# Optimization experiments

Hardware: AMD Instinct MI355X
Metric: run time of the kernel (lower is better)

The kernel has to match this reference:

```python
import jax, jax.numpy as jnp
import numpy as np

ITER_STEPS = 2
NODE_DIM = 512

def _rmv(t, m, value):
    # allennlp.replace_masked_values: keep t where mask nonzero, else value
    return jnp.where(m != 0, t, value)

def setup_inputs() -> dict:
    key = jax.random.key(0)
    ks = jax.random.split(key, 24)
    B, R, C, D, d = 16, 64, 64, 2048, NODE_DIM
    inp = {
        "question_node": jax.random.normal(ks[0], (B, d), jnp.float32),
        "table_row_header_nodes": jax.random.normal(ks[1], (B, R, d), jnp.float32),
        "table_col_header_nodes": jax.random.normal(ks[2], (B, C, d), jnp.float32),
        "table_data_cell_nodes": jax.random.normal(ks[3], (B, D, d), jnp.float32),
        "table_row_header_index_mask": jax.random.randint(ks[4], (B, R), 0, 2, jnp.int32),
        "table_col_header_index_mask": jax.random.randint(ks[5], (B, C), 0, 2, jnp.int32),
        "table_data_cell_index_mask": jax.random.randint(ks[6], (B, D), 0, 2, jnp.int32),
        "same_row_data_cell_relation": jax.random.randint(ks[7], (B, D, D), 0, 2, jnp.int32),
        "same_col_data_cell_relation": jax.random.randint(ks[8], (B, D, D), 0, 2, jnp.int32),
        "data_cell_row_rel": jax.random.randint(ks[9], (B, R, D), 0, 2, jnp.int32),
        "data_cell_col_rel": jax.random.randint(ks[10], (B, C, D), 0, 2, jnp.int32),
        # parameters (Linear(in,out) stores weight [out,in]; y = x @ W.T)
        "w_node": jax.random.normal(ks[11], (1, d), jnp.float32) / np.sqrt(d),
        "w_row_data_cell": jax.random.normal(ks[12], (d, d), jnp.float32) / np.sqrt(d),
        "w_col_data_cell": jax.random.normal(ks[13], (d, d), jnp.float32) / np.sqrt(d),
        "w_data_cell_row": jax.random.normal(ks[14], (d, d), jnp.float32) / np.sqrt(d),
        "w_data_cell_col": jax.random.normal(ks[15], (d, d), jnp.float32) / np.sqrt(d),
        "w_same_row": jax.random.normal(ks[16], (d, d), jnp.float32) / np.sqrt(d),
        "w_same_col": jax.random.normal(ks[17], (d, d), jnp.float32) / np.sqrt(d),
        "w_row_question": jax.random.normal(ks[18], (d, d), jnp.float32) / np.sqrt(d),
        "w_col_question": jax.random.normal(ks[19], (d, d), jnp.float32) / np.sqrt(d),
    }
    return inp


def reference(question_node, table_row_header_nodes, table_col_header_nodes,
              table_data_cell_nodes, table_row_header_index_mask,
              table_col_header_index_mask, table_data_cell_index_mask,
              same_row_data_cell_relation, same_col_data_cell_relation,
              data_cell_row_rel, data_cell_col_rel,
              w_node, w_row_data_cell, w_col_data_cell, w_data_cell_row,
              w_data_cell_col, w_same_row, w_same_col, w_row_question,
              w_col_question):
    rm = table_row_header_index_mask.astype(jnp.float32)   # [B,R]
    cm = table_col_header_index_mask.astype(jnp.float32)   # [B,C]
    dm = table_data_cell_index_mask.astype(jnp.float32)    # [B,D]

    # masked relation graphs (0/1 float)
    rh_dc_graph = data_cell_row_rel.astype(jnp.float32) * (rm[:, :, None] * dm[:, None, :])   # [B,R,D]
    ch_dc_graph = data_cell_col_rel.astype(jnp.float32) * (cm[:, :, None] * dm[:, None, :])   # [B,C,D]
    dc_dc_mask = dm[:, :, None] * dm[:, None, :]
    same_row_graph = same_row_data_cell_relation.astype(jnp.float32) * dc_dc_mask             # [B,D,D]
    same_col_graph = same_col_data_cell_relation.astype(jnp.float32) * dc_dc_mask             # [B,D,D]

    rh_num = rh_dc_graph.sum(-1)                                  # [B,R]
    rh_num = _rmv(rh_num + 1.0, (rh_num >= 1), 1.0)
    ch_num = ch_dc_graph.sum(-1)                                  # [B,C]
    ch_num = _rmv(ch_num + 1.0, (ch_num >= 1), 1.0)
    dc_num = (same_row_graph.sum(-1) + same_col_graph.sum(-1)
              + rh_dc_graph.sum(1) + ch_dc_graph.sum(1))          # [B,D]
    dc_num = _rmv(dc_num, (dc_num >= 1), 1.0)

    rh = table_row_header_nodes
    ch = table_col_header_nodes
    dc = table_data_cell_nodes
    q = question_node

    for _ in range(ITER_STEPS):
        rh_w = jax.nn.sigmoid(rh @ w_node.T)[..., 0]   # [B,R]
        ch_w = jax.nn.sigmoid(ch @ w_node.T)[..., 0]   # [B,C]
        dc_w = jax.nn.sigmoid(dc @ w_node.T)[..., 0]   # [B,D]

        rh_dc_info = dc @ w_row_data_cell.T            # [B,D,d]
        ch_dc_info = dc @ w_col_data_cell.T            # [B,D,d]
        rh_q_info = (q @ w_row_question.T)[:, None, :] * rm[:, :, None]  # [B,R,d]
        ch_q_info = (q @ w_col_question.T)[:, None, :] * cm[:, :, None]  # [B,C,d]
        same_row_info = dc @ w_same_row.T              # [B,D,d]
        same_col_info = dc @ w_same_col.T              # [B,D,d]
        dc_rh_info = rh @ w_data_cell_row.T            # [B,R,d]
        dc_ch_info = ch @ w_data_cell_col.T            # [B,C,d]

        # gated adjacency weights: source-node sigmoid gate masked by graph
        rh_dc_weight = jnp.where(rh_dc_graph != 0, dc_w[:, None, :], 0.0)         # [B,R,D]
        ch_dc_weight = jnp.where(ch_dc_graph != 0, dc_w[:, None, :], 0.0)         # [B,C,D]
        same_row_weight = jnp.where(same_row_graph != 0, dc_w[:, None, :], 0.0)   # [B,D,D]
        same_col_weight = jnp.where(same_col_graph != 0, dc_w[:, None, :], 0.0)   # [B,D,D]
        dc_rh_weight = jnp.where(jnp.swapaxes(rh_dc_graph, 1, 2) != 0, rh_w[:, None, :], 0.0)  # [B,D,R]
        dc_ch_weight = jnp.where(jnp.swapaxes(ch_dc_graph, 1, 2) != 0, ch_w[:, None, :], 0.0)  # [B,D,C]

        rh_dc_agg = jnp.matmul(rh_dc_weight, rh_dc_info)        # [B,R,d]
        ch_dc_agg = jnp.matmul(ch_dc_weight, ch_dc_info)        # [B,C,d]
        same_row_agg = jnp.matmul(same_row_weight, same_row_info)  # [B,D,d]
        same_col_agg = jnp.matmul(same_col_weight, same_col_info)  # [B,D,d]
        dc_rh_agg = jnp.matmul(dc_rh_weight, dc_rh_info)        # [B,D,d]
        dc_ch_agg = jnp.matmul(dc_ch_weight, dc_ch_info)        # [B,D,d]

        agg_rh = (rh_dc_agg + rh_q_info) / rh_num[:, :, None]
        agg_ch = (ch_dc_agg + ch_q_info) / ch_num[:, :, None]
        # NOTE: faithful to source bug: dc_ch_agg appears twice, same_col_agg unused
        agg_dc = (same_row_agg + dc_ch_agg + dc_rh_agg + dc_ch_agg) / dc_num[:, :, None]

        rh = jax.nn.relu(agg_rh)
        ch = jax.nn.relu(agg_ch)
        dc = jax.nn.relu(agg_dc)

    return (rh, ch, dc)
```

## Files before the change

kernel.cpp:

```cpp
#include <hip/hip_runtime.h>
#include <math.h>

#define NB 16
#define NR 64
#define NCOL 64
#define ND 2048
#define DIM 512

typedef __attribute__((ext_vector_type(4))) float f32x4;
typedef __attribute__((ext_vector_type(8))) short bf16x8;
typedef __attribute__((ext_vector_type(8))) unsigned short us8;

#define OFF_RHNUM  0L
#define OFF_CHNUM  1024L
#define OFF_DCNUM  2048L
#define OFF_RHW    34816L
#define OFF_CHW    35840L
#define OFF_QROW   36864L
#define OFF_QCOL   45056L
#define OFF_PRER   53248L
#define OFF_PREC   577536L
#define OFF_INFORC 1101824L
#define OFF_BITS   2150400L
#define OFF_DCS    4247552L
#define OFF_PROJ   21024768L
#define WS_FLOATS  37801984L

__device__ inline void bsplit(float v, unsigned short& h, unsigned short& l) {
    unsigned uv = __float_as_uint(v);
    unsigned hb = (uv + 0x7FFFu + ((uv >> 16) & 1u)) >> 16;
    h = (unsigned short)hb;
    float lo = v - __uint_as_float(hb << 16);
    unsigned lv = __float_as_uint(lo);
    l = (unsigned short)((lv + 0x7FFFu + ((lv >> 16) & 1u)) >> 16);
}

__device__ inline unsigned spread4(unsigned x) {
    x = (x | (x << 12)) & 0x000F000Fu;
    x = (x | (x << 6))  & 0x03030303u;
    x = (x | (x << 3))  & 0x11111111u;
    return x;
}

__device__ inline void mfma_phase2(const unsigned short* Aexp, const unsigned short* Bhi,
                                   const unsigned short* Blo, int wm, int wn, int lane,
                                   f32x4 acc[4][4])
{
    #pragma unroll
    for (int ks = 0; ks < 2; ks++) {
        bf16x8 af[4], bh[4], bl[4];
        #pragma unroll
        for (int i = 0; i < 4; i++) {
            int rr = wm * 64 + i * 16 + (lane & 15);
            int cc = (ks * 4 + (lane >> 4)) ^ (rr & 7);
            af[i] = *(const bf16x8*)((const char*)Aexp + rr * 128 + cc * 16);
            int nn = wn * 64 + i * 16 + (lane & 15);
            int c2 = (ks * 4 + (lane >> 4)) ^ (nn & 7);
            bh[i] = *(const bf16x8*)((const char*)Bhi + nn * 128 + c2 * 16);
            bl[i] = *(const bf16x8*)((const char*)Blo + nn * 128 + c2 * 16);
        }
        #pragma unroll
        for (int mi = 0; mi < 4; mi++)
            #pragma unroll
            for (int ni = 0; ni < 4; ni++) {
                acc[mi][ni] = __builtin_amdgcn_mfma_f32_16x16x32_bf16(af[mi], bh[ni], acc[mi][ni], 0, 0, 0);
                acc[mi][ni] = __builtin_amdgcn_mfma_f32_16x16x32_bf16(af[mi], bl[ni], acc[mi][ni], 0, 0, 0);
            }
    }
}

__global__ __launch_bounds__(256) void k_gate_rc(
    const float* __restrict__ rh, const float* __restrict__ ch,
    const int* __restrict__ rm, const int* __restrict__ cm,
    const float* __restrict__ wnode,
    float* __restrict__ rh_w, float* __restrict__ ch_w)
{
    int wave = threadIdx.x >> 6, lane = threadIdx.x & 63;
    int idx = blockIdx.x * 4 + wave;
    const float* xrow; float* outw; int mval;
    if (idx < NB * NR) {
        int b = idx >> 6, r = idx & 63;
        xrow = rh + ((long)b * NR + r) * DIM; mval = rm[b * NR + r]; outw = rh_w + b * NR + r;
    } else {
        int tt = idx - NB * NR; int b = tt >> 6, c = tt & 63;
        xrow = ch + ((long)b * NCOL + c) * DIM; mval = cm[b * NCOL + c]; outw = ch_w + b * NCOL + c;
    }
    const float4* px = (const float4*)xrow;
    const float4* pw = (const float4*)wnode;
    float4 xa = px[lane * 2], xb = px[lane * 2 + 1];
    float4 wa = pw[lane * 2], wb = pw[lane * 2 + 1];
    float s = xa.x * wa.x + xa.y * wa.y + xa.z * wa.z + xa.w * wa.w
            + xb.x * wb.x + xb.y * wb.y + xb.z * wb.z + xb.w * wb.w;
    #pragma unroll
    for (int o = 32; o > 0; o >>= 1) s += __shfl_xor(s, o, 64);
    if (lane == 0) {
        float g = 1.f / (1.f + expf(-s));
        *outw = mval ? g : 0.f;
    }
}

__global__ __launch_bounds__(256) void k_split(
    const float* __restrict__ src, const float* __restrict__ wnode, const int* __restrict__ dmask,
    unsigned short* __restrict__ dhi, unsigned short* __restrict__ dlo,
    unsigned short* __restrict__ thi, unsigned short* __restrict__ tlo)
{
    int b = blockIdx.y, j0 = blockIdx.x * 16;
    __shared__ float X[16 * 512];
    __shared__ float scs[16];
    int t = threadIdx.x;
    int r = t >> 4, u = t & 15;
    const float* row = src + ((long)b * ND + j0 + r) * DIM;
    float part = 0.f;
    #pragma unroll
    for (int i = 0; i < 8; i++) {
        int col = i * 64 + u * 4;
        float4 v = *(const float4*)(row + col);
        float4 w = *(const float4*)(wnode + col);
        part += v.x * w.x + v.y * w.y + v.z * w.z + v.w * w.w;
        *(float4*)&X[r * 512 + (col ^ ((r & 7) * 4))] = v;
    }
    part += __shfl_xor(part, 1, 64);
    part += __shfl_xor(part, 2, 64);
    part += __shfl_xor(part, 4, 64);
    part += __shfl_xor(part, 8, 64);
    if (u == 0) {
        float g = 1.f / (1.f + expf(-part));
        scs[r] = (dmask[(long)b * ND + j0 + r] != 0) ? g : 0.f;
    }
    __syncthreads();
    {
        float s = scs[r];
        long ob = ((long)b * ND + j0 + r) * DIM + u * 32;
        #pragma unroll
        for (int g = 0; g < 4; g++) {
            us8 ph, pl;
            #pragma unroll
            for (int e = 0; e < 8; e++) {
                int cc = u * 32 + g * 8 + e;
                float v = X[r * 512 + (cc ^ ((r & 7) * 4))] * s;
                unsigned short hh, ll; bsplit(v, hh, ll);
                ph[e] = hh; pl[e] = ll;
            }
            *(us8*)(dhi + ob + g * 8) = ph;
            *(us8*)(dlo + ob + g * 8) = pl;
        }
    }
    #pragma unroll
    for (int h = 0; h < 2; h++) {
        int n = t + h * 256;
        us8 ph0, ph1, pl0, pl1;
        #pragma unroll
        for (int rr = 0; rr < 16; rr++) {
            float v = X[rr * 512 + (n ^ ((rr & 7) * 4))] * scs[rr];
            unsigned short hh, ll; bsplit(v, hh, ll);
            if (rr < 8) { ph0[rr] = hh; pl0[rr] = ll; }
            else        { ph1[rr - 8] = hh; pl1[rr - 8] = ll; }
        }
        long ob = ((long)b * DIM + n) * ND + j0;
        *(us8*)(thi + ob) = ph0; *(us8*)(thi + ob + 8) = ph1;
        *(us8*)(tlo + ob) = pl0; *(us8*)(tlo + ob + 8) = pl1;
    }
}

__global__ __launch_bounds__(256) void k_wsplit(
    const float* __restrict__ w, unsigned short* __restrict__ whi, unsigned short* __restrict__ wlo)
{
    long i = ((long)blockIdx.x * 256 + threadIdx.x) * 8;
    float4 a = *(const float4*)(w + i), b4 = *(const float4*)(w + i + 4);
    float v[8] = {a.x, a.y, a.z, a.w, b4.x, b4.y, b4.z, b4.w};
    us8 ph, pl;
    #pragma unroll
    for (int t = 0; t < 8; t++) {
        unsigned short hh, ll; bsplit(v[t], hh, ll);
        ph[t] = hh; pl[t] = ll;
    }
    *(us8*)(whi + i) = ph;
    *(us8*)(wlo + i) = pl;
}

__global__ __launch_bounds__(256) void k_q(
    const float* __restrict__ q, const float* __restrict__ wrq, const float* __restrict__ wcq,
    float* __restrict__ qrow, float* __restrict__ qcol)
{
    int b = blockIdx.z;
    const float* W = blockIdx.y ? wcq : wrq;
    float* out = blockIdx.y ? qcol : qrow;
    int wave = threadIdx.x >> 6, lane = threadIdx.x & 63;
    int n = blockIdx.x * 4 + wave;
    const float4* qp = (const float4*)(q + (long)b * DIM);
    const float4* wp = (const float4*)(W + (long)n * DIM);
    float4 a0 = qp[lane * 2], a1 = qp[lane * 2 + 1];
    float4 w0 = wp[lane * 2], w1 = wp[lane * 2 + 1];
    float s = a0.x * w0.x + a0.y * w0.y + a0.z * w0.z + a0.w * w0.w
            + a1.x * w1.x + a1.y * w1.y + a1.z * w1.z + a1.w * w1.w;
    #pragma unroll
    for (int o = 32; o > 0; o >>= 1) s += __shfl_xor(s, o, 64);
    if (lane == 0) out[(long)b * DIM + n] = s;
}

__global__ __launch_bounds__(256) void k_bits(
    const int* __restrict__ sr, const int* __restrict__ sc, const int* __restrict__ dmask,
    unsigned* __restrict__ bits, float* __restrict__ dcnum)
{
    long bi0 = (long)blockIdx.x * 2;
    int b = (int)(bi0 >> 11);
    int wave = threadIdx.x >> 6, lane = threadIdx.x & 63;
    const int4* dm4 = (const int4*)(dmask + (long)b * ND);
    int4 vs[2][2], vc[2][2], vd[2];
    #pragma unroll
    for (int h = 0; h < 2; h++) {
        int vidx = wave * 128 + h * 64 + lane;
        vd[h] = dm4[vidx];
        #pragma unroll
        for (int r = 0; r < 2; r++) {
            vs[r][h] = ((const int4*)(sr + (bi0 + r) * ND))[vidx];
            vc[r][h] = ((const int4*)(sc + (bi0 + r) * ND))[vidx];
        }
    }
    int dmi0 = dmask[bi0], dmi1 = dmask[bi0 + 1];
    __shared__ int red[2][4];
    #pragma unroll
    for (int r = 0; r < 2; r++) {
        int dmi = r ? dmi1 : dmi0;
        unsigned* brow = bits + (bi0 + r) * 64;
        int cnt = 0;
        #pragma unroll
        for (int h = 0; h < 2; h++) {
            int4 s4 = vs[r][h], c4 = vc[r][h], d4 = vd[h];
            bool d0 = dmi && d4.x, d1 = dmi && d4.y, d2 = dmi && d4.z, d3 = dmi && d4.w;
            unsigned long long m0 = __ballot(d0 && s4.x);
            unsigned long long m1 = __ballot(d1 && s4.y);
            unsigned long long m2 = __ballot(d2 && s4.z);
            unsigned long long m3 = __ballot(d3 && s4.w);
            unsigned long long n0 = __ballot(d0 && c4.x);
            unsigned long long n1 = __ballot(d1 && c4.y);
            unsigned long long n2 = __ballot(d2 && c4.z);
            unsigned long long n3 = __ballot(d3 && c4.w);
            cnt += __popcll(m0) + __popcll(m1) + __popcll(m2) + __popcll(m3)
                 + __popcll(n0) + __popcll(n1) + __popcll(n2) + __popcll(n3);
            if (lane < 8) {
                unsigned w = spread4((unsigned)(m0 >> (8 * lane)) & 0xFFu)
                           | (spread4((unsigned)(m1 >> (8 * lane)) & 0xFFu) << 1)
                           | (spread4((unsigned)(m2 >> (8 * lane)) & 0xFFu) << 2)
                           | (spread4((unsigned)(m3 >> (8 * lane)) & 0xFFu) << 3);
                brow[wave * 16 + h * 8 + lane] = w;
            }
        }
        if (lane == 0) red[r][wave] = cnt;
    }
    __syncthreads();
    if (threadIdx.x < 2) {
        int s = red[threadIdx.x][0] + red[threadIdx.x][1] + red[threadIdx.x][2] + red[threadIdx.x][3];
        dcnum[bi0 + threadIdx.x] = (float)s;
    }
}

__global__ __launch_bounds__(256) void k_rcnum(
    const int* __restrict__ rel_rd, const int* __restrict__ rel_cd,
    const int* __restrict__ rm, const int* __restrict__ cm, const int* __restrict__ dmask,
    float* __restrict__ rh_num, float* __restrict__ ch_num)
{
    int wave = threadIdx.x >> 6, lane = threadIdx.x & 63;
    long idx = (long)blockIdx.x * 4 + wave;
    const int* row; int mval; float* out; const int* dmb;
    if (idx < NB * NR) {
        int b = (int)(idx >> 6), r = (int)(idx & 63);
        row = rel_rd + ((long)b * NR + r) * ND; mval = rm[b * NR + r];
        out = rh_num + b * NR + r; dmb = dmask + (long)b * ND;
    } else {
        long tt = idx - NB * NR; int b = (int)(tt >> 6), c = (int)(tt & 63);
        row = rel_cd + ((long)b * NCOL + c) * ND; mval = cm[b * NCOL + c];
        out = ch_num + b * NCOL + c; dmb = dmask + (long)b * ND;
    }
    int cnt = 0;
    for (int rr = 0; rr < 32; rr++) {
        int j = rr * 64 + lane;
        cnt += (row[j] != 0 && dmb[j] != 0) ? 1 : 0;
    }
    #pragma unroll
    for (int o = 32; o > 0; o >>= 1) cnt += __shfl_xor(cnt, o, 64);
    if (lane == 0) {
        float s = mval ? (float)cnt : 0.f;
        *out = (s >= 1.f) ? (s + 1.f) : 1.f;
    }
}

__global__ __launch_bounds__(256) void k_dcnum_final(
    const int* __restrict__ rel_rd, const int* __restrict__ rel_cd,
    const int* __restrict__ rm, const int* __restrict__ cm, const int* __restrict__ dmask,
    float* __restrict__ dcnum)
{
    int b = blockIdx.y;
    int j = blockIdx.x * 256 + threadIdx.x;
    const int* rd = rel_rd + (long)b * NR * ND;
    const int* cd = rel_cd + (long)b * NCOL * ND;
    const int* rmb = rm + b * NR;
    const int* cmb = cm + b * NCOL;
    int cnt = 0;
    for (int r = 0; r < NR; r++)  cnt += (rd[(long)r * ND + j] != 0 && rmb[r] != 0) ? 1 : 0;
    for (int c = 0; c < NCOL; c++) cnt += (cd[(long)c * ND + j] != 0 && cmb[c] != 0) ? 1 : 0;
    float add = (dmask[(long)b * ND + j] != 0) ? (float)cnt : 0.f;
    float tv = dcnum[(long)b * ND + j] + add;
    dcnum[(long)b * ND + j] = (tv >= 1.f) ? tv : 1.f;
}

__global__ __launch_bounds__(256) void gemm_info(
    const float* __restrict__ A, long sA,
    const float* __restrict__ W,
    unsigned short* __restrict__ ihiT, unsigned short* __restrict__ iloT, int hoff,
    const float* __restrict__ rowscale, float alpha)
{
    int b = blockIdx.z;
    int n0 = blockIdx.x * 64;
    __shared__ float As[32][68], Ws[32][68];
    float acc[4][4] = {};
    int tx = threadIdx.x & 15, ty = threadIdx.x >> 4;
    int lm = threadIdx.x >> 2, lk = (threadIdx.x & 3) * 8;
    const float* Ab = A + (long)b * sA;
    for (int k0 = 0; k0 < DIM; k0 += 32) {
        const float4* pa = (const float4*)(Ab + (long)lm * DIM + k0 + lk);
        float4 va0 = pa[0], va1 = pa[1];
        const float4* pw = (const float4*)(W + (long)(n0 + lm) * DIM + k0 + lk);
        float4 vw0 = pw[0], vw1 = pw[1];
        As[lk + 0][lm] = va0.x; As[lk + 1][lm] = va0.y; As[lk + 2][lm] = va0.z; As[lk + 3][lm] = va0.w;
        As[lk + 4][lm] = va1.x; As[lk + 5][lm] = va1.y; As[lk + 6][lm] = va1.z; As[lk + 7][lm] = va1.w;
        Ws[lk + 0][lm] = vw0.x; Ws[lk + 1][lm] = vw0.y; Ws[lk + 2][lm] = vw0.z; Ws[lk + 3][lm] = vw0.w;
        Ws[lk + 4][lm] = vw1.x; Ws[lk + 5][lm] = vw1.y; Ws[lk + 6][lm] = vw1.z; Ws[lk + 7][lm] = vw1.w;
        __syncthreads();
        #pragma unroll
        for (int kk = 0; kk < 32; kk++) {
            float4 av = *(const float4*)&As[kk][ty * 4];
            float4 wv = *(const float4*)&Ws[kk][tx * 4];
            float a[4] = {av.x, av.y, av.z, av.w};
            float w[4] = {wv.x, wv.y, wv.z, wv.w};
            #pragma unroll
            for (int mi = 0; mi < 4; mi++)
                #pragma unroll
                for (int ni = 0; ni < 4; ni++)
                    acc[mi][ni] += a[mi] * w[ni];
        }
        __syncthreads();
    }
    #pragma unroll
    for (int mi = 0; mi < 4; mi++) {
        int gm = ty * 4 + mi;
        float scv = alpha * rowscale[(long)b * 64 + gm];
        #pragma unroll
        for (int ni = 0; ni < 4; ni++) {
            float v = scv * acc[mi][ni];
            unsigned short hh, ll; bsplit(v, hh, ll);
            long off = ((long)b * DIM + n0 + tx * 4 + ni) * 128 + hoff + gm;
            ihiT[off] = hh; iloT[off] = ll;
        }
    }
}

__global__ __launch_bounds__(256) void gemm_head(
    const float* __restrict__ A, long sA,
    const float* __restrict__ W,
    float* __restrict__ C, long sC,
    const int* __restrict__ mrow, const float* __restrict__ addvec,
    const float* __restrict__ rownum)
{
    int b = blockIdx.z;
    int n0 = blockIdx.x * 64;
    __shared__ float As[32][68], Ws[32][68];
    float acc[4][4] = {};
    int tx = threadIdx.x & 15, ty = threadIdx.x >> 4;
    int lm = threadIdx.x >> 2, lk = (threadIdx.x & 3) * 8;
    const float* Ab = A + (long)b * sA;
    for (int k0 = 0; k0 < DIM; k0 += 32) {
        const float4* pa = (const float4*)(Ab + (long)lm * DIM + k0 + lk);
        float4 va0 = pa[0], va1 = pa[1];
        const float4* pw = (const float4*)(W + (long)(n0 + lm) * DIM + k0 + lk);
        float4 vw0 = pw[0], vw1 = pw[1];
        As[lk + 0][lm] = va0.x; As[lk + 1][lm] = va0.y; As[lk + 2][lm] = va0.z; As[lk + 3][lm] = va0.w;
        As[lk + 4][lm] = va1.x; As[lk + 5][lm] = va1.y; As[lk + 6][lm] = va1.z; As[lk + 7][lm] = va1.w;
        Ws[lk + 0][lm] = vw0.x; Ws[lk + 1][lm] = vw0.y; Ws[lk + 2][lm] = vw0.z; Ws[lk + 3][lm] = vw0.w;
        Ws[lk + 4][lm] = vw1.x; Ws[lk + 5][lm] = vw1.y; Ws[lk + 6][lm] = vw1.z; Ws[lk + 7][lm] = vw1.w;
        __syncthreads();
        #pragma unroll
        for (int kk = 0; kk < 32; kk++) {
            float4 av = *(const float4*)&As[kk][ty * 4];
            float4 wv = *(const float4*)&Ws[kk][tx * 4];
            float a[4] = {av.x, av.y, av.z, av.w};
            float w[4] = {wv.x, wv.y, wv.z, wv.w};
            #pragma unroll
            for (int mi = 0; mi < 4; mi++)
                #pragma unroll
                for (int ni = 0; ni < 4; ni++)
                    acc[mi][ni] += a[mi] * w[ni];
        }
        __syncthreads();
    }
    #pragma unroll
    for (int mi = 0; mi < 4; mi++) {
        int gm = ty * 4 + mi;
        float mq = (mrow[(long)b * 64 + gm] != 0) ? 1.f : 0.f;
        float inv = 1.f / rownum[(long)b * 64 + gm];
        float4 o;
        float* vo = (float*)&o;
        #pragma unroll
        for (int ni = 0; ni < 4; ni++) {
            float tv = (acc[mi][ni] + mq * addvec[(long)b * DIM + n0 + tx * 4 + ni]) * inv;
            vo[ni] = fmaxf(tv, 0.f);
        }
        *(float4*)(C + (long)b * sC + (long)gm * DIM + n0 + tx * 4) = o;
    }
}

__global__ __launch_bounds__(256) void k_pre_rc_mfma(
    const int* __restrict__ rel_rd, const int* __restrict__ rel_cd,
    const unsigned short* __restrict__ thi, const unsigned short* __restrict__ tlo,
    const int* __restrict__ rm, const int* __restrict__ cm,
    float* __restrict__ pre_r, float* __restrict__ pre_c)
{
    int b = blockIdx.y, n0 = blockIdx.x * 64;
    __shared__ unsigned short Aexp[128 * 64];
    __shared__ unsigned short Bhi[64 * 64], Blo[64 * 64];
    int tid = threadIdx.x, lane = tid & 63, wid = tid >> 6;
    int wm = wid >> 1, wn = wid & 1;
    int arow = tid >> 1, aseg = tid & 1;
    const int* relrow = (arow < 64)
        ? rel_rd + ((long)b * 64 + arow) * ND
        : rel_cd + ((long)b * 64 + arow - 64) * ND;
    int bn = tid >> 2, bq = tid & 3;
    const unsigned short* bsrc_h = thi + ((long)b * DIM + n0 + bn) * ND;
    const unsigned short* bsrc_l = tlo + ((long)b * DIM + n0 + bn) * ND;

    f32x4 acc[4][2];
    #pragma unroll
    for (int i = 0; i < 4; i++)
        #pragma unroll
        for (int j = 0; j < 2; j++)
            acc[i][j] = (f32x4){0.f, 0.f, 0.f, 0.f};

    for (int k0 = 0; k0 < ND; k0 += 64) {
        {
            const int4* pa = (const int4*)(relrow + k0 + aseg * 32);
            #pragma unroll
            for (int p = 0; p < 4; p++) {
                int4 v0 = pa[2 * p], v1 = pa[2 * p + 1];
                uint4 qv;
                qv.x = (v0.x ? 0x3F80u : 0u) | (v0.y ? 0x3F800000u : 0u);
                qv.y = (v0.z ? 0x3F80u : 0u) | (v0.w ? 0x3F800000u : 0u);
                qv.z = (v1.x ? 0x3F80u : 0u) | (v1.y ? 0x3F800000u : 0u);
                qv.w = (v1.z ? 0x3F80u : 0u) | (v1.w ? 0x3F800000u : 0u);
                int c = (aseg * 4 + p) ^ (arow & 7);
                *(uint4*)((char*)Aexp + arow * 128 + c * 16) = qv;
            }
        }
        {
            const uint4* ph = (const uint4*)(bsrc_h + k0 + bq * 16);
            const uint4* pl = (const uint4*)(bsrc_l + k0 + bq * 16);
            #pragma unroll
            for (int s = 0; s < 2; s++) {
                int c = (bq * 2 + s) ^ (bn & 7);
                *(uint4*)((char*)Bhi + bn * 128 + c * 16) = ph[s];
                *(uint4*)((char*)Blo + bn * 128 + c * 16) = pl[s];
            }
        }
        __syncthreads();
        #pragma unroll
        for (int ks = 0; ks < 2; ks++) {
            bf16x8 af[4], bh[2], bl[2];
            #pragma unroll
            for (int i = 0; i < 4; i++) {
                int rr = wm * 64 + i * 16 + (lane & 15);
                int cc = (ks * 4 + (lane >> 4)) ^ (rr & 7);
                af[i] = *(bf16x8*)((char*)Aexp + rr * 128 + cc * 16);
            }
            #pragma unroll
            for (int i = 0; i < 2; i++) {
                int nn = wn * 32 + i * 16 + (lane & 15);
                int c2 = (ks * 4 + (lane >> 4)) ^ (nn & 7);
                bh[i] = *(bf16x8*)((char*)Bhi + nn * 128 + c2 * 16);
                bl[i] = *(bf16x8*)((char*)Blo + nn * 128 + c2 * 16);
            }
            #pragma unroll
            for (int mi = 0; mi < 4; mi++)
                #pragma unroll
                for (int ni = 0; ni < 2; ni++) {
                    acc[mi][ni] = __builtin_amdgcn_mfma_f32_16x16x32_bf16(af[mi], bh[ni], acc[mi][ni], 0, 0, 0);
                    acc[mi][ni] = __builtin_amdgcn_mfma_f32_16x16x32_bf16(af[mi], bl[ni], acc[mi][ni], 0, 0, 0);
                }
        }
        __syncthreads();
    }
    const int* msk = wm ? cm : rm;
    float* outp = wm ? pre_c : pre_r;
    #pragma unroll
    for (int mi = 0; mi < 4; mi++) {
        int grow = mi * 16 + (lane >> 4) * 4;
        #pragma unroll
        for (int ni = 0; ni < 2; ni++) {
            int gcol = n0 + wn * 32 + ni * 16 + (lane & 15);
            #pragma unroll
            for (int r = 0; r < 4; r++) {
                int rrow = grow + r;
                float scv = (msk[b * 64 + rrow] != 0) ? 1.f : 0.f;
                outp[((long)b * 64 + rrow) * DIM + gcol] = scv * acc[mi][ni][r];
            }
        }
    }
}

__global__ __launch_bounds__(256) void k_proj_mfma(
    const unsigned short* __restrict__ whi, const unsigned short* __restrict__ wlo,
    const unsigned short* __restrict__ dhi, const unsigned short* __restrict__ dlo,
    unsigned short* __restrict__ phi, unsigned short* __restrict__ plo)
{
    int flat = blockIdx.x;
    int tile = (flat & 7) * 128 + (flat >> 3);
    int b = tile >> 6;
    int rem = tile & 63;
    int m0 = (rem >> 4) * 128;
    int n0 = (rem & 15) * 128;

    __shared__ unsigned short SM[4 * 128 * 64];
    unsigned short* Ahi = SM;
    unsigned short* Alo = SM + 128 * 64;
    unsigned short* Bhi = SM + 2 * 128 * 64;
    unsigned short* Blo = SM + 3 * 128 * 64;

    int tid = threadIdx.x;
    int lane = tid & 63, wid = tid >> 6;
    int wm = wid >> 1, wn = wid & 1;
    int srow = tid >> 1, sseg = tid & 1;

    f32x4 acc[4][4];
    #pragma unroll
    for (int i = 0; i < 4; i++)
        #pragma unroll
        for (int j = 0; j < 4; j++)
            acc[i][j] = (f32x4){0.f, 0.f, 0.f, 0.f};

    for (int k0 = 0; k0 < DIM; k0 += 64) {
        {
            const uint4* ph = (const uint4*)(whi + (long)(m0 + srow) * DIM + k0 + sseg * 32);
            const uint4* pl = (const uint4*)(wlo + (long)(m0 + srow) * DIM + k0 + sseg * 32);
            #pragma unroll
            for (int s = 0; s < 4; s++) {
                int c = (sseg * 4 + s) ^ (srow & 7);
                *(uint4*)((char*)Ahi + srow * 128 + c * 16) = ph[s];
                *(uint4*)((char*)Alo + srow * 128 + c * 16) = pl[s];
            }
        }
        {
            const uint4* ph = (const uint4*)(dhi + ((long)b * ND + n0 + srow) * DIM + k0 + sseg * 32);
            const uint4* pl = (const uint4*)(dlo + ((long)b * ND + n0 + srow) * DIM + k0 + sseg * 32);
            #pragma unroll
            for (int s = 0; s < 4; s++) {
                int c = (sseg * 4 + s) ^ (srow & 7);
                *(uint4*)((char*)Bhi + srow * 128 + c * 16) = ph[s];
                *(uint4*)((char*)Blo + srow * 128 + c * 16) = pl[s];
            }
        }
        __syncthreads();
        #pragma unroll
        for (int ks = 0; ks < 2; ks++) {
            bf16x8 ah[4], al[4], bh[4], bl[4];
            #pragma unroll
            for (int i = 0; i < 4; i++) {
                int rr = wm * 64 + i * 16 + (lane & 15);
                int cc = (ks * 4 + (lane >> 4)) ^ (rr & 7);
                ah[i] = *(bf16x8*)((char*)Ahi + rr * 128 + cc * 16);
                al[i] = *(bf16x8*)((char*)Alo + rr * 128 + cc * 16);
                int nn = wn * 64 + i * 16 + (lane & 15);
                int c2 = (ks * 4 + (lane >> 4)) ^ (nn & 7);
                bh[i] = *(bf16x8*)((char*)Bhi + nn * 128 + c2 * 16);
                bl[i] = *(bf16x8*)((char*)Blo + nn * 128 + c2 * 16);
            }
            #pragma unroll
            for (int mi = 0; mi < 4; mi++)
                #pragma unroll
                for (int ni = 0; ni < 4; ni++) {
                    acc[mi][ni] = __builtin_amdgcn_mfma_f32_16x16x32_bf16(ah[mi], bh[ni], acc[mi][ni], 0, 0, 0);
                    acc[mi][ni] = __builtin_amdgcn_mfma_f32_16x16x32_bf16(ah[mi], bl[ni], acc[mi][ni], 0, 0, 0);
                    acc[mi][ni] = __builtin_amdgcn_mfma_f32_16x16x32_bf16(al[mi], bh[ni], acc[mi][ni], 0, 0, 0);
                }
        }
        __syncthreads();
    }
    unsigned short* Ph = SM;
    unsigned short* Pl = SM + 128 * 128;
    #pragma unroll
    for (int mi = 0; mi < 4; mi++) {
        int lrow = wm * 64 + mi * 16 + (lane >> 4) * 4;
        #pragma unroll
        for (int ni = 0; ni < 4; ni++) {
            int lcol = wn * 64 + ni * 16 + (lane & 15);
            #pragma unroll
            for (int r = 0; r < 4; r++) {
                unsigned short hh, ll; bsplit(acc[mi][ni][r], hh, ll);
                int row = lrow + r;
                int cs = lcol ^ ((row & 3) << 4);
                Ph[row * 128 + cs] = hh;
                Pl[row * 128 + cs] = ll;
            }
        }
    }
    __syncthreads();
    {
        int row = tid >> 1, half = tid & 1;
        long gbase = ((long)b * DIM + m0 + row) * ND + n0 + half * 64;
        int xs = (row & 3) << 4;
        #pragma unroll
        for (int s = 0; s < 8; s++) {
            int col = (half * 64 + s * 8) ^ xs;
            *(us8*)(phi + gbase + s * 8) = *(const us8*)(Ph + row * 128 + col);
            *(us8*)(plo + gbase + s * 8) = *(const us8*)(Pl + row * 128 + col);
        }
    }
}

__global__ __launch_bounds__(256) void k_agg_final(
    const unsigned* __restrict__ bits,
    const unsigned short* __restrict__ phi, const unsigned short* __restrict__ plo,
    const unsigned short* __restrict__ ihiT, const unsigned short* __restrict__ iloT,
    const int* __restrict__ rel_rd, const int* __restrict__ rel_cd,
    const int* __restrict__ dmask, const float* __restrict__ rownum,
    float* __restrict__ out)
{
    int flat = blockIdx.x;
    int tile = (flat & 7) * 128 + (flat >> 3);
    int b = tile >> 6;
    int m0 = ((tile >> 2) & 15) * 128;
    int n0 = (tile & 3) * 128;

    __shared__ unsigned short Aexp[128 * 64];
    __shared__ unsigned short Bhi[128 * 64];
    __shared__ unsigned short Blo[128 * 64];
    __shared__ unsigned short dmu[128];
    __shared__ unsigned LDSw[256];

    int tid = threadIdx.x;
    int lane = tid & 63, wid = tid >> 6;
    int wm = wid >> 1, wn = wid & 1;

    if (tid < 128) dmu[tid] = (dmask[(long)b * ND + m0 + tid] != 0) ? (unsigned short)0x3F80 : (unsigned short)0;

    int arow = tid >> 1, awsel = tid & 1;
    const unsigned* abit_base = bits + ((long)b * ND + m0 + arow) * 64 + awsel;
    char* adst = (char*)Aexp + arow * 128;

    f32x4 acc[4][4];
    #pragma unroll
    for (int i = 0; i < 4; i++)
        #pragma unroll
        for (int j = 0; j < 4; j++)
            acc[i][j] = (f32x4){0.f, 0.f, 0.f, 0.f};

    for (int k0 = 0; k0 < ND; k0 += 64) {
        #pragma unroll
        for (int u = 0; u < 8; u++) {
            int lin = (u & 3) * 256 + tid;
            int n = lin >> 3, c = lin & 7;
            const unsigned short* src = (u < 4 ? phi : plo)
                + ((long)b * DIM + n0 + n) * ND + k0 + c * 8;
            uint4 v = *(const uint4*)src;
            char* dst = (char*)(u < 4 ? Bhi : Blo) + n * 128 + ((c ^ (n & 7)) * 16);
            *(uint4*)dst = v;
        }
        {
            unsigned w = abit_base[k0 >> 5];
            #pragma unroll
            for (int c = 0; c < 4; c++) {
                uint4 qv;
                qv.x = (((w >> (c * 8 + 0)) & 1u) ? 0x3F80u : 0u) | (((w >> (c * 8 + 1)) & 1u) ? 0x3F800000u : 0u);
                qv.y = (((w >> (c * 8 + 2)) & 1u) ? 0x3F80u : 0u) | (((w >> (c * 8 + 3)) & 1u) ? 0x3F800000u : 0u);
                qv.z = (((w >> (c * 8 + 4)) & 1u) ? 0x3F80u : 0u) | (((w >> (c * 8 + 5)) & 1u) ? 0x3F800000u : 0u);
                qv.w = (((w >> (c * 8 + 6)) & 1u) ? 0x3F80u : 0u) | (((w >> (c * 8 + 7)) & 1u) ? 0x3F800000u : 0u);
                int chunk = (awsel * 4 + c) ^ (arow & 7);
                *(uint4*)(adst + chunk * 16) = qv;
            }
        }
        __syncthreads();
        mfma_phase2(Aexp, Bhi, Blo, wm, wn, lane, acc);
        __syncthreads();
    }
    #pragma unroll
    for (int kt = 0; kt < 2; kt++) {
        #pragma unroll
        for (int u = 0; u < 8; u++) {
            int lin = (u & 3) * 256 + tid;
            int n = lin >> 3, c = lin & 7;
            uint4 v = *(const uint4*)((u < 4 ? ihiT : iloT)
                + ((long)b * DIM + n0 + n) * 128 + kt * 64 + c * 8);
            char* dst = (char*)(u < 4 ? Bhi : Blo) + n * 128 + ((c ^ (n & 7)) * 16);
            *(uint4*)dst = v;
        }
        const int* relrow = (kt ? rel_cd : rel_rd) + ((long)b * 64 + lane) * ND + m0 + wid * 32;
        #pragma unroll
        for (int c4 = 0; c4 < 32; c4 += 4) {
            int4 v = *(const int4*)(relrow + c4);
            unsigned long long mm;
            mm = __ballot(v.x != 0);
            if ((lane >> 1) == c4 + 0) LDSw[(wid * 32 + c4 + 0) * 2 + (lane & 1)] = (unsigned)(mm >> ((lane & 1) * 32));
            mm = __ballot(v.y != 0);
            if ((lane >> 1) == c4 + 1) LDSw[(wid * 32 + c4 + 1) * 2 + (lane & 1)] = (unsigned)(mm >> ((lane & 1) * 32));
            mm = __ballot(v.z != 0);
            if ((lane >> 1) == c4 + 2) LDSw[(wid * 32 + c4 + 2) * 2 + (lane & 1)] = (unsigned)(mm >> ((lane & 1) * 32));
            mm = __ballot(v.w != 0);
            if ((lane >> 1) == c4 + 3) LDSw[(wid * 32 + c4 + 3) * 2 + (lane & 1)] = (unsigned)(mm >> ((lane & 1) * 32));
        }
        __syncthreads();
        {
            unsigned w = LDSw[arow * 2 + awsel];
            unsigned dv = (unsigned)dmu[arow];
            unsigned dvh = dv << 16;
            #pragma unroll
            for (int c = 0; c < 4; c++) {
                uint4 qv;
                qv.x = (((w >> (c * 8 + 0)) & 1u) ? dv : 0u) | (((w >> (c * 8 + 1)) & 1u) ? dvh : 0u);
                qv.y = (((w >> (c * 8 + 2)) & 1u) ? dv : 0u) | (((w >> (c * 8 + 3)) & 1u) ? dvh : 0u);
                qv.z = (((w >> (c * 8 + 4)) & 1u) ? dv : 0u) | (((w >> (c * 8 + 5)) & 1u) ? dvh : 0u);
                qv.w = (((w >> (c * 8 + 6)) & 1u) ? dv : 0u) | (((w >> (c * 8 + 7)) & 1u) ? dvh : 0u);
                int chunk = (awsel * 4 + c) ^ (arow & 7);
                *(uint4*)(adst + chunk * 16) = qv;
            }
        }
        __syncthreads();
        mfma_phase2(Aexp, Bhi, Blo, wm, wn, lane, acc);
        __syncthreads();
    }
    #pragma unroll
    for (int mi = 0; mi < 4; mi++) {
        int grow = m0 + wm * 64 + mi * 16 + (lane >> 4) * 4;
        float inv[4];
        #pragma unroll
        for (int r = 0; r < 4; r++) inv[r] = 1.f / rownum[(long)b * ND + grow + r];
        #pragma unroll
        for (int ni = 0; ni < 4; ni++) {
            int gcol = n0 + wn * 64 + ni * 16 + (lane & 15);
            #pragma unroll
            for (int r = 0; r < 4; r++) {
                long off = ((long)b * ND + grow + r) * DIM + gcol;
                out[off] = fmaxf(acc[mi][ni][r] * inv[r], 0.f);
            }
        }
    }
}

extern "C" void kernel_launch(void* const* d_in, const int* in_sizes, int n_in,
                              void* d_out, int out_size, void* d_ws, size_t ws_size,
                              hipStream_t stream)
{
    const float* q       = (const float*)d_in[0];
    const float* rh0     = (const float*)d_in[1];
    const float* ch0     = (const float*)d_in[2];
    const float* dc0     = (const float*)d_in[3];
    const int*   rm      = (const int*)d_in[4];
    const int*   cm      = (const int*)d_in[5];
    const int*   dmask   = (const int*)d_in[6];
    const int*   same_row= (const int*)d_in[7];
    const int*   same_col= (const int*)d_in[8];
    const int*   rel_rd  = (const int*)d_in[9];
    const int*   rel_cd  = (const int*)d_in[10];
    const float* wnode   = (const float*)d_in[11];
    const float* w_rdc   = (const float*)d_in[12];
    const float* w_cdc   = (const float*)d_in[13];
    const float* w_dcr   = (const float*)d_in[14];
    const float* w_dcc   = (const float*)d_in[15];
    const float* w_sr    = (const float*)d_in[16];
    const float* w_rq    = (const float*)d_in[18];
    const float* w_cq    = (const float*)d_in[19];

    float* out = (float*)d_out;
    float* rh = out;
    float* ch = out + (long)NB * NR * DIM;
    float* dc = out + (long)NB * NR * DIM * 2;

    if (ws_size < (size_t)WS_FLOATS * 4) return;

    float* ws      = (float*)d_ws;
    float* rh_num  = ws + OFF_RHNUM;
    float* ch_num  = ws + OFF_CHNUM;
    float* dc_num  = ws + OFF_DCNUM;
    float* rh_w    = ws + OFF_RHW;
    float* ch_w    = ws + OFF_CHW;
    float* qrow    = ws + OFF_QROW;
    float* qcol    = ws + OFF_QCOL;
    float* pre_r   = ws + OFF_PRER;
    float* pre_c   = ws + OFF_PREC;
    unsigned short* ihiT = (unsigned short*)(ws + OFF_INFORC);
    unsigned short* iloT = ihiT + (size_t)NB * DIM * 128;
    unsigned* bits = (unsigned*)(ws + OFF_BITS);
    unsigned short* dhi = (unsigned short*)(ws + OFF_DCS);
    unsigned short* dlo = dhi + (size_t)NB * ND * DIM;
    unsigned short* thi = (unsigned short*)(ws + OFF_PROJ);
    unsigned short* tlo = thi + (size_t)NB * DIM * ND;
    unsigned short* phi = (unsigned short*)(ws + OFF_PROJ);
    unsigned short* plo = phi + (size_t)NB * DIM * ND;
    unsigned short* whi = (unsigned short*)dc;
    unsigned short* wlo = whi + (size_t)DIM * DIM;

    hipMemcpyAsync(rh, rh0, sizeof(float) * (size_t)NB * NR * DIM, hipMemcpyDeviceToDevice, stream);
    hipMemcpyAsync(ch, ch0, sizeof(float) * (size_t)NB * NCOL * DIM, hipMemcpyDeviceToDevice, stream);

    k_bits<<<NB * ND / 2, 256, 0, stream>>>(same_row, same_col, dmask, bits, dc_num);
    k_rcnum<<<512, 256, 0, stream>>>(rel_rd, rel_cd, rm, cm, dmask, rh_num, ch_num);
    k_dcnum_final<<<dim3(ND / 256, NB), 256, 0, stream>>>(rel_rd, rel_cd, rm, cm, dmask, dc_num);
    k_q<<<dim3(128, 2, NB), 256, 0, stream>>>(q, w_rq, w_cq, qrow, qcol);

    for (int it = 0; it < 2; it++) {
        k_gate_rc<<<512, 256, 0, stream>>>(rh, ch, rm, cm, wnode, rh_w, ch_w);
        k_split<<<dim3(128, NB), 256, 0, stream>>>(it == 0 ? dc0 : dc, wnode, dmask, dhi, dlo, thi, tlo);
        k_wsplit<<<128, 256, 0, stream>>>(w_sr, whi, wlo);
        gemm_info<<<dim3(8, 1, NB), 256, 0, stream>>>(rh, (long)NR * DIM, w_dcr,
            ihiT, iloT, 0, rh_w, 1.0f);
        gemm_info<<<dim3(8, 1, NB), 256, 0, stream>>>(ch, (long)NCOL * DIM, w_dcc,
            ihiT, iloT, 64, ch_w, 2.0f);
        k_pre_rc_mfma<<<dim3(8, NB), 256, 0, stream>>>(rel_rd, rel_cd, thi, tlo, rm, cm, pre_r, pre_c);
        k_proj_mfma<<<1024, 256, 0, stream>>>(whi, wlo, dhi, dlo, phi, plo);
        gemm_head<<<dim3(8, 1, NB), 256, 0, stream>>>(pre_r, (long)NR * DIM, w_rdc,
            rh, (long)NR * DIM, rm, qrow, rh_num);
        gemm_head<<<dim3(8, 1, NB), 256, 0, stream>>>(pre_c, (long)NCOL * DIM, w_cdc,
            ch, (long)NCOL * DIM, cm, qcol, ch_num);
        k_agg_final<<<1024, 256, 0, stream>>>(bits, phi, plo, ihiT, iloT,
            rel_rd, rel_cd, dmask, dc_num, dc);
    }
}
```

Before: 1.145 ms.

## Use direct global-to-LDS loads for GEMM tiles and drop LDS-staged projection stores

Replaces the register-staged global→LDS tile copies in the projection and aggregation kernels with global_load_lds 16-byte direct loads. The XOR swizzle moves from the LDS destination onto the global source address so the MFMA read layout stays the same. The projection epilogue now writes hi/lo bf16 halves straight to global memory with scalar 2-byte stores instead of staging through LDS. This aims to cut VGPR pressure and load/store instruction count in the main loops. The price is uncoalesced short stores in the epilogue and a dependence on the hardware ordering of direct-to-LDS loads before the barrier.

```diff
diff --git a/kernel.cpp b/kernel.cpp
--- a/kernel.cpp
+++ b/kernel.cpp
@@ -10,6 +10,10 @@
 typedef __attribute__((ext_vector_type(4))) float f32x4;
 typedef __attribute__((ext_vector_type(8))) short bf16x8;
 typedef __attribute__((ext_vector_type(8))) unsigned short us8;
+
+#define GLD(src, dst) __builtin_amdgcn_global_load_lds( \
+    (const __attribute__((address_space(1))) void*)(src), \
+    (__attribute__((address_space(3))) void*)(dst), 16, 0, 0)
 
 #define OFF_RHNUM  0L
 #define OFF_CHNUM  1024L
@@ -517,16 +521,31 @@
     int m0 = (rem >> 4) * 128;
     int n0 = (rem & 15) * 128;
 
-    __shared__ unsigned short SM[4 * 128 * 64];
-    unsigned short* Ahi = SM;
-    unsigned short* Alo = SM + 128 * 64;
-    unsigned short* Bhi = SM + 2 * 128 * 64;
-    unsigned short* Blo = SM + 3 * 128 * 64;
+    __shared__ unsigned short Ahi[128 * 64], Alo[128 * 64];
+    __shared__ unsigned short Bhi[128 * 64], Blo[128 * 64];
 
     int tid = threadIdx.x;
     int lane = tid & 63, wid = tid >> 6;
     int wm = wid >> 1, wn = wid & 1;
-    int srow = tid >> 1, sseg = tid & 1;
+
+    long ro0, ro1, ro2, ro3;
+    {
+        int L = wid * 64 + lane;
+        int n = L >> 3, cg = (L & 7) ^ (n & 7);
+        ro0 = (long)n * DIM + cg * 8;
+        L += 256; n = L >> 3; cg = (L & 7) ^ (n & 7);
+        ro1 = (long)n * DIM + cg * 8;
+        L += 256; n = L >> 3; cg = (L & 7) ^ (n & 7);
+        ro2 = (long)n * DIM + cg * 8;
+        L += 256; n = L >> 3; cg = (L & 7) ^ (n & 7);
+        ro3 = (long)n * DIM + cg * 8;
+    }
+    const unsigned short* wh_b = whi + (long)m0 * DIM;
+    const unsigned short* wl_b = wlo + (long)m0 * DIM;
+    const unsigned short* dh_b = dhi + ((long)b * ND + n0) * DIM;
+    const unsigned short* dl_b = dlo + ((long)b * ND + n0) * DIM;
+    int lb0 = (wid * 64) * 8, lb1 = (256 + wid * 64) * 8,
+        lb2 = (512 + wid * 64) * 8, lb3 = (768 + wid * 64) * 8;
 
     f32x4 acc[4][4];
     #pragma unroll
@@ -536,26 +555,14 @@
             acc[i][j] = (f32x4){0.f, 0.f, 0.f, 0.f};
 
     for (int k0 = 0; k0 < DIM; k0 += 64) {
-        {
-            const uint4* ph = (const uint4*)(whi + (long)(m0 + srow) * DIM + k0 + sseg * 32);
-            const uint4* pl = (const uint4*)(wlo + (long)(m0 + srow) * DIM + k0 + sseg * 32);
-            #pragma unroll
-            for (int s = 0; s < 4; s++) {
-                int c = (sseg * 4 + s) ^ (srow & 7);
-                *(uint4*)((char*)Ahi + srow * 128 + c * 16) = ph[s];
-                *(uint4*)((char*)Alo + srow * 128 + c * 16) = pl[s];
-            }
-        }
-        {
-            const uint4* ph = (const uint4*)(dhi + ((long)b * ND + n0 + srow) * DIM + k0 + sseg * 32);
-            const uint4* pl = (const uint4*)(dlo + ((long)b * ND + n0 + srow) * DIM + k0 + sseg * 32);
-            #pragma unroll
-            for (int s = 0; s < 4; s++) {
-                int c = (sseg * 4 + s) ^ (srow & 7);
-                *(uint4*)((char*)Bhi + srow * 128 + c * 16) = ph[s];
-                *(uint4*)((char*)Blo + srow * 128 + c * 16) = pl[s];
-            }
-        }
+        GLD(wh_b + ro0 + k0, Ahi + lb0); GLD(wh_b + ro1 + k0, Ahi + lb1);
+        GLD(wh_b + ro2 + k0, Ahi + lb2); GLD(wh_b + ro3 + k0, Ahi + lb3);
+        GLD(wl_b + ro0 + k0, Alo + lb0); GLD(wl_b + ro1 + k0, Alo + lb1);
+        GLD(wl_b + ro2 + k0, Alo + lb2); GLD(wl_b + ro3 + k0, Alo + lb3);
+        GLD(dh_b + ro0 + k0, Bhi + lb0); GLD(dh_b + ro1 + k0, Bhi + lb1);
+        GLD(dh_b + ro2 + k0, Bhi + lb2); GLD(dh_b + ro3 + k0, Bhi + lb3);
+        GLD(dl_b + ro0 + k0, Blo + lb0); GLD(dl_b + ro1 + k0, Blo + lb1);
+        GLD(dl_b + ro2 + k0, Blo + lb2); GLD(dl_b + ro3 + k0, Blo + lb3);
         __syncthreads();
         #pragma unroll
         for (int ks = 0; ks < 2; ks++) {
@@ -582,34 +589,18 @@
         }
         __syncthreads();
     }
-    unsigned short* Ph = SM;
-    unsigned short* Pl = SM + 128 * 128;
     #pragma unroll
     for (int mi = 0; mi < 4; mi++) {
-        int lrow = wm * 64 + mi * 16 + (lane >> 4) * 4;
+        int grow = m0 + wm * 64 + mi * 16 + (lane >> 4) * 4;
         #pragma unroll
         for (int ni = 0; ni < 4; ni++) {
-            int lcol = wn * 64 + ni * 16 + (lane & 15);
+            int gcol = n0 + wn * 64 + ni * 16 + (lane & 15);
             #pragma unroll
             for (int r = 0; r < 4; r++) {
                 unsigned short hh, ll; bsplit(acc[mi][ni][r], hh, ll);
-                int row = lrow + r;
-                int cs = lcol ^ ((row & 3) << 4);
-                Ph[row * 128 + cs] = hh;
-                Pl[row * 128 + cs] = ll;
-            }
-        }
-    }
-    __syncthreads();
-    {
-        int row = tid >> 1, half = tid & 1;
-        long gbase = ((long)b * DIM + m0 + row) * ND + n0 + half * 64;
-        int xs = (row & 3) << 4;
-        #pragma unroll
-        for (int s = 0; s < 8; s++) {
-            int col = (half * 64 + s * 8) ^ xs;
-            *(us8*)(phi + gbase + s * 8) = *(const us8*)(Ph + row * 128 + col);
-            *(us8*)(plo + gbase + s * 8) = *(const us8*)(Pl + row * 128 + col);
+                long off = ((long)b * DIM + grow + r) * ND + gcol;
+                phi[off] = hh; plo[off] = ll;
+            }
         }
     }
 }
@@ -644,6 +635,24 @@
     const unsigned* abit_base = bits + ((long)b * ND + m0 + arow) * 64 + awsel;
     char* adst = (char*)Aexp + arow * 128;
 
+    long bo0, bo1, bo2, bo3;
+    long io0, io1, io2, io3;
+    {
+        int L = wid * 64 + lane;
+        int n = L >> 3, cg = (L & 7) ^ (n & 7);
+        bo0 = (long)n * ND + cg * 8;  io0 = (long)n * 128 + cg * 8;
+        L += 256; n = L >> 3; cg = (L & 7) ^ (n & 7);
+        bo1 = (long)n * ND + cg * 8;  io1 = (long)n * 128 + cg * 8;
+        L += 256; n = L >> 3; cg = (L & 7) ^ (n & 7);
+        bo2 = (long)n * ND + cg * 8;  io2 = (long)n * 128 + cg * 8;
+        L += 256; n = L >> 3; cg = (L & 7) ^ (n & 7);
+        bo3 = (long)n * ND + cg * 8;  io3 = (long)n * 128 + cg * 8;
+    }
+    const unsigned short* ph_b = phi + ((long)b * DIM + n0) * ND;
+    const unsigned short* pl_b = plo + ((long)b * DIM + n0) * ND;
+    int lb0 = (wid * 64) * 8, lb1 = (256 + wid * 64) * 8,
+        lb2 = (512 + wid * 64) * 8, lb3 = (768 + wid * 64) * 8;
+
     f32x4 acc[4][4];
     #pragma unroll
     for (int i = 0; i < 4; i++)
@@ -652,16 +661,10 @@
             acc[i][j] = (f32x4){0.f, 0.f, 0.f, 0.f};
 
     for (int k0 = 0; k0 < ND; k0 += 64) {
-        #pragma unroll
-        for (int u = 0; u < 8; u++) {
-            int lin = (u & 3) * 256 + tid;
-            int n = lin >> 3, c = lin & 7;
-            const unsigned short* src = (u < 4 ? phi : plo)
-                + ((long)b * DIM + n0 + n) * ND + k0 + c * 8;
-            uint4 v = *(const uint4*)src;
-            char* dst = (char*)(u < 4 ? Bhi : Blo) + n * 128 + ((c ^ (n & 7)) * 16);
-            *(uint4*)dst = v;
-        }
+        GLD(ph_b + bo0 + k0, Bhi + lb0); GLD(ph_b + bo1 + k0, Bhi + lb1);
+        GLD(ph_b + bo2 + k0, Bhi + lb2); GLD(ph_b + bo3 + k0, Bhi + lb3);
+        GLD(pl_b + bo0 + k0, Blo + lb0); GLD(pl_b + bo1 + k0, Blo + lb1);
+        GLD(pl_b + bo2 + k0, Blo + lb2); GLD(pl_b + bo3 + k0, Blo + lb3);
         {
             unsigned w = abit_base[k0 >> 5];
             #pragma unroll
@@ -681,15 +684,12 @@
     }
     #pragma unroll
     for (int kt = 0; kt < 2; kt++) {
-        #pragma unroll
-        for (int u = 0; u < 8; u++) {
-            int lin = (u & 3) * 256 + tid;
-            int n = lin >> 3, c = lin & 7;
-            uint4 v = *(const uint4*)((u < 4 ? ihiT : iloT)
-                + ((long)b * DIM + n0 + n) * 128 + kt * 64 + c * 8);
-            char* dst = (char*)(u < 4 ? Bhi : Blo) + n * 128 + ((c ^ (n & 7)) * 16);
-            *(uint4*)dst = v;
-        }
+        const unsigned short* ih_b = ihiT + ((long)b * DIM + n0) * 128 + kt * 64;
+        const unsigned short* il_b = iloT + ((long)b * DIM + n0) * 128 + kt * 64;
+        GLD(ih_b + io0, Bhi + lb0); GLD(ih_b + io1, Bhi + lb1);
+        GLD(ih_b + io2, Bhi + lb2); GLD(ih_b + io3, Bhi + lb3);
+        GLD(il_b + io0, Blo + lb0); GLD(il_b + io1, Blo + lb1);
+        GLD(il_b + io2, Blo + lb2); GLD(il_b + io3, Blo + lb3);
         const int* relrow = (kt ? rel_cd : rel_rd) + ((long)b * 64 + lane) * ND + m0 + wid * 32;
         #pragma unroll
         for (int c4 = 0; c4 < 32; c4 += 4) {
```

New measurement: 1.074 ms. -6.2%, faster.
